# Optimization experiments

Measured on AMD Instinct MI355X. Metric: run time of the kernel, lower is better.

## Reference

```python
import jax, jax.numpy as jnp
import numpy as np

TOPK = 2
EPS = 1e-6  # RMSNorm epsilon


def setup_inputs() -> dict:
    key = jax.random.key(0)
    ks = jax.random.split(key, 8)
    b, t, d, h, n = 2, 1024, 1024, 2048, 16
    x = jax.random.normal(ks[0], (b, t, d), dtype=jnp.float32)
    router_w = jax.random.normal(ks[1], (n, d), dtype=jnp.float32) * (1.0 / np.sqrt(d))
    router_bias = jnp.zeros((n,), dtype=jnp.float32)
    bank_mag = jax.random.normal(ks[2], (n, d, h), dtype=jnp.float32) * (1.0 / np.sqrt(d))
    bank_freq = jax.random.uniform(ks[3], (n, d, h), dtype=jnp.float32, minval=0.5, maxval=2.0) * (1.0 / np.sqrt(d))
    bank_phase = jax.random.uniform(ks[4], (n, h), dtype=jnp.float32, minval=-0.3, maxval=0.3)
    bank_down = jax.random.normal(ks[5], (n, h, d), dtype=jnp.float32) * (1.0 / np.sqrt(h))
    norm_w = jnp.ones((d,), dtype=jnp.float32)
    return {
        'x': x, 'router_w': router_w, 'router_bias': router_bias,
        'bank_mag': bank_mag, 'bank_freq': bank_freq, 'bank_phase': bank_phase,
        'bank_down': bank_down, 'norm_w': norm_w,
    }


def reference(x, router_w, router_bias, bank_mag, bank_freq, bank_phase, bank_down, norm_w):
    b, t, d = x.shape
    # Router: scores [b,t,n], top-k selection, softmax over selected logits
    scores = jnp.einsum('btd,nd->btn', x, router_w) + router_bias
    topv, topi = jax.lax.top_k(scores, TOPK)            # [b,t,k]
    weights = jax.nn.softmax(topv, axis=-1)             # [b,t,k]

    fx = x.reshape(b * t, d)                            # [T,d]
    # Dense per-expert compute (mathematically identical to per-token gather+bmm):
    mag = jnp.einsum('td,ndh->tnh', fx, bank_mag)       # [T,n,h]
    freq = jnp.einsum('td,ndh->tnh', fx, bank_freq)     # [T,n,h]
    hidden = jnp.tanh(mag) * jnp.cos(jax.nn.softplus(freq) + 0.1 + bank_phase[None, :, :])
    out_all = jnp.einsum('tnh,nhd->tnd', hidden, bank_down)  # [T,n,d]

    # Gather the top-k expert outputs per token and combine with routing weights
    ti = topi.reshape(b * t, TOPK)                      # [T,k]
    sel = jnp.take_along_axis(out_all, ti[:, :, None], axis=1)  # [T,k,d]
    out = jnp.einsum('tkd,tk->td', sel, weights.reshape(b * t, TOPK)).reshape(b, t, d)

    # RMSNorm
    out = out * jax.lax.rsqrt(jnp.mean(out * out, axis=-1, keepdims=True) + EPS) * norm_w
    return out
```

## Files before the change

### kernel.cpp

```cpp
#include <hip/hip_runtime.h>
#include <hip/hip_bf16.h>
#include <cstdint>
#include <cstddef>

#define TT 2048
#define DD 1024
#define HH 2048
#define NE 16
#define WM128 48
#define BROW 17

typedef __bf16 bf16x8 __attribute__((ext_vector_type(8)));
typedef float f32x4 __attribute__((ext_vector_type(4)));

__device__ __forceinline__ unsigned short f2bf(float f) {
  union { float f; unsigned u; } v; v.f = f;
  unsigned r = (v.u + 0x7FFFu + ((v.u >> 16) & 1u)) >> 16;
  return (unsigned short)r;
}
__device__ __forceinline__ float bf2f(unsigned short s) {
  union { unsigned u; float f; } v; v.u = ((unsigned)s) << 16;
  return v.f;
}
__device__ __forceinline__ unsigned packbf(float lo, float hi) {
  return (unsigned)f2bf(lo) | ((unsigned)f2bf(hi) << 16);
}

__device__ __forceinline__ void gl_lds16(const void* g, void* l) {
  __builtin_amdgcn_global_load_lds(
      (const __attribute__((address_space(1))) unsigned int*)g,
      (__attribute__((address_space(3))) unsigned int*)l, 16, 0, 0);
}

union U4 { unsigned int u[4]; bf16x8 v; };

#define BARRIER_N(N)                                            \
  do {                                                          \
    asm volatile("s_waitcnt vmcnt(" #N ")" ::: "memory");       \
    asm volatile("s_waitcnt lgkmcnt(0)" ::: "memory");          \
    __builtin_amdgcn_sched_barrier(0);                          \
    __builtin_amdgcn_s_barrier();                               \
    __builtin_amdgcn_sched_barrier(0);                          \
  } while (0)

__global__ __launch_bounds__(256) void k_router(
    const float* __restrict__ x, const float* __restrict__ rw,
    const float* __restrict__ rb, int* __restrict__ cnt,
    int* __restrict__ list_tok, int* __restrict__ rec,
    float* __restrict__ wrec, unsigned short* __restrict__ xbf) {
  const int t = blockIdx.x;
  __shared__ float xs[DD];
  __shared__ float part[256];
  __shared__ float sc[NE];
  const float* xr = x + (size_t)t * DD;
  for (int i = threadIdx.x; i < DD; i += 256) xs[i] = xr[i];
  __syncthreads();
  {
    int i = threadIdx.x * 4;
    ushort4 o = { f2bf(xs[i]), f2bf(xs[i + 1]), f2bf(xs[i + 2]), f2bf(xs[i + 3]) };
    *reinterpret_cast<ushort4*>(xbf + (size_t)t * DD + i) = o;
  }
  const int e = threadIdx.x >> 4, j = threadIdx.x & 15;
  const float* w = rw + (size_t)e * DD;
  float s = 0.f;
  for (int i = j; i < DD; i += 16) s += xs[i] * w[i];
  part[threadIdx.x] = s;
  __syncthreads();
  if (threadIdx.x < NE) {
    float v = rb[threadIdx.x];
    #pragma unroll
    for (int q = 0; q < 16; ++q) v += part[threadIdx.x * 16 + q];
    sc[threadIdx.x] = v;
  }
  __syncthreads();
  if (threadIdx.x == 0) {
    int e1 = 0; float v1 = sc[0];
    #pragma unroll
    for (int q = 1; q < NE; ++q) { if (sc[q] > v1) { v1 = sc[q]; e1 = q; } }
    int e2 = -1; float v2 = -3.4e38f;
    #pragma unroll
    for (int q = 0; q < NE; ++q) {
      if (q != e1 && sc[q] > v2) { v2 = sc[q]; e2 = q; }
    }
    float ex = expf(v2 - v1);
    float w1 = 1.f / (1.f + ex);
    float w2 = ex / (1.f + ex);
    int p1 = atomicAdd(&cnt[e1], 1);
    int p2 = atomicAdd(&cnt[e2], 1);
    list_tok[e1 * TT + p1] = t;
    list_tok[e2 * TT + p2] = t;
    rec[t * 4 + 0] = e1; rec[t * 4 + 1] = p1;
    rec[t * 4 + 2] = e2; rec[t * 4 + 3] = p2;
    wrec[t * 2 + 0] = w1; wrec[t * 2 + 1] = w2;
  }
}

__global__ void k_sched(const int* __restrict__ cnt, int* __restrict__ work128,
                        int* __restrict__ woff) {
  if (threadIdx.x == 0) {
    int o = 0, n1 = 0;
    for (int e = 0; e < NE; ++e) {
      int ce = cnt[e];
      int a = (ce + 127) >> 7;
      for (int mb = 0; mb < a; ++mb) { work128[n1 * 2] = e; work128[n1 * 2 + 1] = mb; ++n1; }
      woff[e] = o; o += ce;
    }
    for (int q = n1; q < WM128; ++q) { work128[q * 2] = -1; work128[q * 2 + 1] = 0; }
  }
}

__global__ __launch_bounds__(256, 3) void k_up(
    const unsigned short* __restrict__ xbf,
    const float* __restrict__ bmag,
    const float* __restrict__ bfreq,
    const float* __restrict__ bphase,
    const int* __restrict__ cnt, const int* __restrict__ list_tok,
    const int* __restrict__ work, const int* __restrict__ woff,
    unsigned short* __restrict__ hid) {
  const int e = work[blockIdx.x * 2 + 0];
  if (e < 0) return;
  const int mt = work[blockIdx.x * 2 + 1];
  const int nt = blockIdx.y;
  const int ce = cnt[e];
  const int off = woff[e];
  __shared__ unsigned short As[2][128][32];
  __shared__ unsigned int BuM[2][64 * BROW];
  __shared__ unsigned int BuF[2][64 * BROW];
  __shared__ int toks[128];
  const int tid = threadIdx.x;
  if (tid < 128) {
    int r = mt * 128 + tid;
    toks[tid] = list_tok[e * TT + (r < ce ? r : ce - 1)];
  }
  __syncthreads();
  const int w = tid >> 6, l = tid & 63;
  size_t abase[2]; int aoff[2];
  #pragma unroll
  for (int p = 0; p < 2; ++p) {
    int row = p * 64 + w * 16 + (l >> 2);
    int g = (l & 3) ^ ((row >> 1) & 3);
    abase[p] = (size_t)toks[row] * DD + g * 8;
    aoff[p] = (p * 256 + w * 64 + l) * 8;
  }
  const int q2 = tid >> 4;
  const int b16 = tid & 15;
  const int n0 = nt * 64;
  const float* srcM = bmag  + (size_t)e * DD * HH + n0 + 4 * b16;
  const float* srcF = bfreq + (size_t)e * DD * HH + n0 + 4 * b16;
  int bwv[4];
  #pragma unroll
  for (int i = 0; i < 4; ++i) bwv[i] = (4 * b16 + i) * BROW + q2;

  const int wm = (w >> 1) * 64, wn = (w & 1) * 32;
  const int lr = l & 15, kg = l >> 4;
  const f32x4 zero = {0.f, 0.f, 0.f, 0.f};
  f32x4 accM[4][2], accF[4][2];
  #pragma unroll
  for (int a = 0; a < 4; ++a)
    #pragma unroll
    for (int b = 0; b < 2; ++b) { accM[a][b] = zero; accF[a][b] = zero; }

  float4 Am0, Am1, Af0, Af1;
  float4 Bm0, Bm1, Bf0, Bf1;

  auto glA = [&](int kt, int buf) {
    #pragma unroll
    for (int j = 0; j < 2; ++j)
      gl_lds16(xbf + abase[j] + kt * 32, &As[buf][0][0] + aoff[j]);
  };
  auto loadBA = [&](int kt) {
    const float* pM = srcM + (size_t)(kt * 32 + 2 * q2) * HH;
    const float* pF = srcF + (size_t)(kt * 32 + 2 * q2) * HH;
    Am0 = *reinterpret_cast<const float4*>(pM);
    Am1 = *reinterpret_cast<const float4*>(pM + HH);
    Af0 = *reinterpret_cast<const float4*>(pF);
    Af1 = *reinterpret_cast<const float4*>(pF + HH);
  };
  auto loadBB = [&](int kt) {
    const float* pM = srcM + (size_t)(kt * 32 + 2 * q2) * HH;
    const float* pF = srcF + (size_t)(kt * 32 + 2 * q2) * HH;
    Bm0 = *reinterpret_cast<const float4*>(pM);
    Bm1 = *reinterpret_cast<const float4*>(pM + HH);
    Bf0 = *reinterpret_cast<const float4*>(pF);
    Bf1 = *reinterpret_cast<const float4*>(pF + HH);
  };
  auto writeBA = [&](int buf) {
    const float* m0 = reinterpret_cast<const float*>(&Am0);
    const float* m1 = reinterpret_cast<const float*>(&Am1);
    const float* f0 = reinterpret_cast<const float*>(&Af0);
    const float* f1 = reinterpret_cast<const float*>(&Af1);
    #pragma unroll
    for (int i = 0; i < 4; ++i) {
      BuM[buf][bwv[i]] = packbf(m0[i], m1[i]);
      BuF[buf][bwv[i]] = packbf(f0[i], f1[i]);
    }
  };
  auto writeBB = [&](int buf) {
    const float* m0 = reinterpret_cast<const float*>(&Bm0);
    const float* m1 = reinterpret_cast<const float*>(&Bm1);
    const float* f0 = reinterpret_cast<const float*>(&Bf0);
    const float* f1 = reinterpret_cast<const float*>(&Bf1);
    #pragma unroll
    for (int i = 0; i < 4; ++i) {
      BuM[buf][bwv[i]] = packbf(m0[i], m1[i]);
      BuF[buf][bwv[i]] = packbf(f0[i], f1[i]);
    }
  };
  auto compute = [&](int buf) {
    bf16x8 av[4];
    #pragma unroll
    for (int fm = 0; fm < 4; ++fm) {
      int row = wm + fm * 16 + lr;
      int c = kg ^ ((row >> 1) & 3);
      av[fm] = *reinterpret_cast<const bf16x8*>(&As[buf][row][c * 8]);
    }
    U4 tm[2], tf[2];
    #pragma unroll
    for (int fn = 0; fn < 2; ++fn) {
      const int nb = (wn + fn * 16 + lr) * BROW + kg * 4;
      #pragma unroll
      for (int j2 = 0; j2 < 4; ++j2) {
        tm[fn].u[j2] = BuM[buf][nb + j2];
        tf[fn].u[j2] = BuF[buf][nb + j2];
      }
    }
    #pragma unroll
    for (int fm = 0; fm < 4; ++fm)
      #pragma unroll
      for (int fn = 0; fn < 2; ++fn) {
        accM[fm][fn] = __builtin_amdgcn_mfma_f32_16x16x32_bf16(av[fm], tm[fn].v, accM[fm][fn], 0, 0, 0);
        accF[fm][fn] = __builtin_amdgcn_mfma_f32_16x16x32_bf16(av[fm], tf[fn].v, accF[fm][fn], 0, 0, 0);
      }
  };

  glA(0, 0);
  __builtin_amdgcn_sched_barrier(0);
  loadBA(0);
  loadBB(1);
  writeBA(0);
  BARRIER_N(4);
  for (int kt = 0; kt < 32; kt += 2) {
    glA(kt + 1, 1);
    __builtin_amdgcn_sched_barrier(0);
    loadBA(kt + 2 < 32 ? kt + 2 : 31);
    compute(0);
    writeBB(1);
    BARRIER_N(4);
    const bool more = kt + 2 < 32;
    if (more) {
      glA(kt + 2, 0);
      __builtin_amdgcn_sched_barrier(0);
      loadBB(kt + 3 < 32 ? kt + 3 : 31);
    }
    compute(1);
    if (more) {
      writeBA(0);
      BARRIER_N(4);
    }
  }
  #pragma unroll
  for (int fn = 0; fn < 2; ++fn) {
    const int ng = n0 + wn + fn * 16 + lr;
    const float ph = bphase[e * HH + ng] + 0.1f;
    #pragma unroll
    for (int fm = 0; fm < 4; ++fm) {
      #pragma unroll
      for (int jj = 0; jj < 4; ++jj) {
        int m = mt * 128 + wm + fm * 16 + kg * 4 + jj;
        if (m < ce) {
          float mv = accM[fm][fn][jj];
          float fv = accF[fm][fn][jj];
          float exn = __expf(-fabsf(fv));
          float sp = fmaxf(fv, 0.f) + __logf(1.f + exn);
          float t2 = __expf(2.f * mv);
          float th = 1.f - 2.f / (t2 + 1.f);
          float hv = th * __cosf(sp + ph);
          hid[(size_t)(off + m) * HH + ng] = f2bf(hv);
        }
      }
    }
  }
}

__global__ __launch_bounds__(256, 4) void k_down(
    const unsigned short* __restrict__ hid,
    const float* __restrict__ bdown,
    const int* __restrict__ cnt,
    const int* __restrict__ work, const int* __restrict__ woff,
    unsigned short* __restrict__ op) {
  const int e = work[blockIdx.x * 2 + 0];
  if (e < 0) return;
  const int mt = work[blockIdx.x * 2 + 1];
  const int nt = blockIdx.y;
  const int ce = cnt[e];
  const int off = woff[e];
  __shared__ unsigned short As[2][128][32];
  __shared__ unsigned int Bu[2][64 * BROW];
  const int tid = threadIdx.x;
  const int w = tid >> 6, l = tid & 63;
  size_t abase[2]; int aoff[2];
  #pragma unroll
  for (int p = 0; p < 2; ++p) {
    int row = p * 64 + w * 16 + (l >> 2);
    int g = (l & 3) ^ ((row >> 1) & 3);
    int gr = mt * 128 + row; if (gr >= ce) gr = ce - 1;
    abase[p] = (size_t)(off + gr) * HH + g * 8;
    aoff[p] = (p * 256 + w * 64 + l) * 8;
  }
  const int q2 = tid >> 4;
  const int b16 = tid & 15;
  const int n0 = nt * 64;
  const float* srcD = bdown + (size_t)e * HH * DD + n0 + 4 * b16;
  int bwv[4];
  #pragma unroll
  for (int i = 0; i < 4; ++i) bwv[i] = (4 * b16 + i) * BROW + q2;

  const int wm = (w >> 1) * 64, wn = (w & 1) * 32;
  const int lr = l & 15, kg = l >> 4;
  const f32x4 zero = {0.f, 0.f, 0.f, 0.f};
  f32x4 acc[4][2];
  #pragma unroll
  for (int a = 0; a < 4; ++a)
    #pragma unroll
    for (int b = 0; b < 2; ++b) acc[a][b] = zero;

  float4 Ad0, Ad1;
  float4 Bd0, Bd1;

  auto glA = [&](int kt, int buf) {
    #pragma unroll
    for (int j = 0; j < 2; ++j)
      gl_lds16(hid + abase[j] + kt * 32, &As[buf][0][0] + aoff[j]);
  };
  auto loadBA = [&](int kt) {
    const float* pD = srcD + (size_t)(kt * 32 + 2 * q2) * DD;
    Ad0 = *reinterpret_cast<const float4*>(pD);
    Ad1 = *reinterpret_cast<const float4*>(pD + DD);
  };
  auto loadBB = [&](int kt) {
    const float* pD = srcD + (size_t)(kt * 32 + 2 * q2) * DD;
    Bd0 = *reinterpret_cast<const float4*>(pD);
    Bd1 = *reinterpret_cast<const float4*>(pD + DD);
  };
  auto writeBA = [&](int buf) {
    const float* d0 = reinterpret_cast<const float*>(&Ad0);
    const float* d1 = reinterpret_cast<const float*>(&Ad1);
    #pragma unroll
    for (int i = 0; i < 4; ++i) Bu[buf][bwv[i]] = packbf(d0[i], d1[i]);
  };
  auto writeBB = [&](int buf) {
    const float* d0 = reinterpret_cast<const float*>(&Bd0);
    const float* d1 = reinterpret_cast<const float*>(&Bd1);
    #pragma unroll
    for (int i = 0; i < 4; ++i) Bu[buf][bwv[i]] = packbf(d0[i], d1[i]);
  };
  auto compute = [&](int buf) {
    bf16x8 av[4];
    #pragma unroll
    for (int fm = 0; fm < 4; ++fm) {
      int row = wm + fm * 16 + lr;
      int c = kg ^ ((row >> 1) & 3);
      av[fm] = *reinterpret_cast<const bf16x8*>(&As[buf][row][c * 8]);
    }
    U4 t[2];
    #pragma unroll
    for (int fn = 0; fn < 2; ++fn) {
      const int nb = (wn + fn * 16 + lr) * BROW + kg * 4;
      #pragma unroll
      for (int j2 = 0; j2 < 4; ++j2) t[fn].u[j2] = Bu[buf][nb + j2];
    }
    #pragma unroll
    for (int fm = 0; fm < 4; ++fm)
      #pragma unroll
      for (int fn = 0; fn < 2; ++fn)
        acc[fm][fn] = __builtin_amdgcn_mfma_f32_16x16x32_bf16(av[fm], t[fn].v, acc[fm][fn], 0, 0, 0);
  };

  glA(0, 0);
  __builtin_amdgcn_sched_barrier(0);
  loadBA(0);
  loadBB(1);
  writeBA(0);
  BARRIER_N(2);
  for (int kt = 0; kt < 64; kt += 2) {
    glA(kt + 1, 1);
    __builtin_amdgcn_sched_barrier(0);
    loadBA(kt + 2 < 64 ? kt + 2 : 63);
    compute(0);
    writeBB(1);
    BARRIER_N(2);
    const bool more = kt + 2 < 64;
    if (more) {
      glA(kt + 2, 0);
      __builtin_amdgcn_sched_barrier(0);
      loadBB(kt + 3 < 64 ? kt + 3 : 63);
    }
    compute(1);
    if (more) {
      writeBA(0);
      BARRIER_N(2);
    }
  }
  #pragma unroll
  for (int fn = 0; fn < 2; ++fn) {
    const int ng = n0 + wn + fn * 16 + lr;
    #pragma unroll
    for (int fm = 0; fm < 4; ++fm) {
      #pragma unroll
      for (int jj = 0; jj < 4; ++jj) {
        int m = mt * 128 + wm + fm * 16 + kg * 4 + jj;
        if (m < ce)
          op[(size_t)(off + m) * DD + ng] = f2bf(acc[fm][fn][jj]);
      }
    }
  }
}

__global__ __launch_bounds__(256) void k_norm(
    const unsigned short* __restrict__ op, const int* __restrict__ woff,
    const int* __restrict__ rec, const float* __restrict__ wrec,
    const float* __restrict__ nw, float* __restrict__ out) {
  const int t = blockIdx.x;
  const int tid = threadIdx.x;
  __shared__ float red[4];
  const int e1 = rec[t * 4 + 0], p1 = rec[t * 4 + 1];
  const int e2 = rec[t * 4 + 2], p2 = rec[t * 4 + 3];
  const float w1 = wrec[t * 2 + 0], w2 = wrec[t * 2 + 1];
  const unsigned short* pa = op + (size_t)(woff[e1] + p1) * DD;
  const unsigned short* pb = op + (size_t)(woff[e2] + p2) * DD;
  float v[4]; float ss = 0.f;
  #pragma unroll
  for (int q = 0; q < 4; ++q) {
    int i = q * 256 + tid;
    v[q] = w1 * bf2f(pa[i]) + w2 * bf2f(pb[i]);
    ss += v[q] * v[q];
  }
  #pragma unroll
  for (int o = 32; o > 0; o >>= 1) ss += __shfl_xor(ss, o);
  if ((tid & 63) == 0) red[tid >> 6] = ss;
  __syncthreads();
  const float tot = red[0] + red[1] + red[2] + red[3];
  const float scl = rsqrtf(tot * (1.f / DD) + 1e-6f);
  #pragma unroll
  for (int q = 0; q < 4; ++q) {
    int i = q * 256 + tid;
    out[(size_t)t * DD + i] = v[q] * scl * nw[i];
  }
}

extern "C" void kernel_launch(void* const* d_in, const int* in_sizes, int n_in,
                              void* d_out, int out_size, void* d_ws, size_t ws_size,
                              hipStream_t stream) {
  const float* x      = (const float*)d_in[0];
  const float* rw     = (const float*)d_in[1];
  const float* rb     = (const float*)d_in[2];
  const float* bmag   = (const float*)d_in[3];
  const float* bfreq  = (const float*)d_in[4];
  const float* bphase = (const float*)d_in[5];
  const float* bdown  = (const float*)d_in[6];
  const float* nw     = (const float*)d_in[7];
  float* out = (float*)d_out;
  char* ws = (char*)d_ws;
  const size_t MB = 1024 * 1024;
  int*   cnt    = (int*)(ws + 0);
  int*   work1  = (int*)(ws + 128);
  int*   woff   = (int*)(ws + 2048);
  int*   list   = (int*)(ws + 4096);
  int*   rec    = (int*)(ws + 139264);
  float* wrec   = (float*)(ws + 172032);
  unsigned short* xbf = (unsigned short*)(ws + 1 * MB);
  unsigned short* hid = (unsigned short*)(ws + 5 * MB);
  unsigned short* op  = (unsigned short*)(ws + 21 * MB);

  hipMemsetAsync(cnt, 0, 64, stream);
  k_router<<<TT, 256, 0, stream>>>(x, rw, rb, cnt, list, rec, wrec, xbf);
  k_sched<<<1, 64, 0, stream>>>(cnt, work1, woff);
  k_up<<<dim3(WM128, HH / 64), 256, 0, stream>>>(xbf, bmag, bfreq, bphase,
                                                 cnt, list, work1, woff, hid);
  k_down<<<dim3(WM128, DD / 64), 256, 0, stream>>>(hid, bdown, cnt, work1, woff, op);
  k_norm<<<TT, 256, 0, stream>>>(op, woff, rec, wrec, nw, out);
}
```

Baseline: 293.2 us.

## Map expert tiles to XCDs so each expert's weights stay in one L2

Flattens the up and down projection grids to 1D and remaps block indices so that blocks with the same low three bits (which the hardware round-robins onto the same XCD) all work on one or two experts (e and e+8). Each expert's weight slices are then read through a single XCD's L2 instead of being spread across all eight, cutting redundant HBM traffic for the fp32 weight banks. A scheduler flag falls back to the old work-list mapping when some expert pair has too many row tiles to fit the fixed grid. The mapping relies on the round-robin dispatch of workgroups across XCDs and can cause load imbalance between XCDs when experts are uneven.

```diff
diff --git a/kernel.cpp b/kernel.cpp
--- a/kernel.cpp
+++ b/kernel.cpp
@@ -96,16 +96,42 @@
 }
 
 __global__ void k_sched(const int* __restrict__ cnt, int* __restrict__ work128,
-                        int* __restrict__ woff) {
+                        int* __restrict__ woff, int* __restrict__ nmb,
+                        int* __restrict__ flag) {
   if (threadIdx.x == 0) {
     int o = 0, n1 = 0;
     for (int e = 0; e < NE; ++e) {
       int ce = cnt[e];
       int a = (ce + 127) >> 7;
+      nmb[e] = a;
       for (int mb = 0; mb < a; ++mb) { work128[n1 * 2] = e; work128[n1 * 2 + 1] = mb; ++n1; }
       woff[e] = o; o += ce;
     }
     for (int q = n1; q < WM128; ++q) { work128[q * 2] = -1; work128[q * 2 + 1] = 0; }
+    int f = 0;
+    for (int xq = 0; xq < 8; ++xq)
+      if (nmb[xq] + nmb[xq + 8] > 6) f = 1;
+    flag[0] = f;
+  }
+}
+
+__device__ __forceinline__ bool xcd_map(int L, const int* nmb, const int* flag,
+                                        const int* work, int NTSH,
+                                        int& e, int& mt, int& nt) {
+  if (flag[0] == 0) {
+    int x = L & 7, r = L >> 3;
+    int m0 = nmb[x] << NTSH, m1 = nmb[x + 8] << NTSH;
+    if (r < m0) { e = x; mt = r >> NTSH; nt = r & ((1 << NTSH) - 1); return true; }
+    r -= m0;
+    if (r < m1) { e = x + 8; mt = r >> NTSH; nt = r & ((1 << NTSH) - 1); return true; }
+    return false;
+  } else {
+    int wq = L >> NTSH;
+    e = work[wq * 2];
+    if (e < 0) return false;
+    mt = work[wq * 2 + 1];
+    nt = L & ((1 << NTSH) - 1);
+    return true;
   }
 }
 
@@ -116,11 +142,10 @@
     const float* __restrict__ bphase,
     const int* __restrict__ cnt, const int* __restrict__ list_tok,
     const int* __restrict__ work, const int* __restrict__ woff,
+    const int* __restrict__ nmb, const int* __restrict__ flag,
     unsigned short* __restrict__ hid) {
-  const int e = work[blockIdx.x * 2 + 0];
-  if (e < 0) return;
-  const int mt = work[blockIdx.x * 2 + 1];
-  const int nt = blockIdx.y;
+  int e, mt, nt;
+  if (!xcd_map(blockIdx.x, nmb, flag, work, 5, e, mt, nt)) return;
   const int ce = cnt[e];
   const int off = woff[e];
   __shared__ unsigned short As[2][128][32];
@@ -287,11 +312,10 @@
     const float* __restrict__ bdown,
     const int* __restrict__ cnt,
     const int* __restrict__ work, const int* __restrict__ woff,
+    const int* __restrict__ nmb, const int* __restrict__ flag,
     unsigned short* __restrict__ op) {
-  const int e = work[blockIdx.x * 2 + 0];
-  if (e < 0) return;
-  const int mt = work[blockIdx.x * 2 + 1];
-  const int nt = blockIdx.y;
+  int e, mt, nt;
+  if (!xcd_map(blockIdx.x, nmb, flag, work, 4, e, mt, nt)) return;
   const int ce = cnt[e];
   const int off = woff[e];
   __shared__ unsigned short As[2][128][32];
@@ -465,6 +489,8 @@
   int*   cnt    = (int*)(ws + 0);
   int*   work1  = (int*)(ws + 128);
   int*   woff   = (int*)(ws + 2048);
+  int*   nmb    = (int*)(ws + 2176);
+  int*   flag   = (int*)(ws + 2304);
   int*   list   = (int*)(ws + 4096);
   int*   rec    = (int*)(ws + 139264);
   float* wrec   = (float*)(ws + 172032);
@@ -474,9 +500,9 @@
 
   hipMemsetAsync(cnt, 0, 64, stream);
   k_router<<<TT, 256, 0, stream>>>(x, rw, rb, cnt, list, rec, wrec, xbf);
-  k_sched<<<1, 64, 0, stream>>>(cnt, work1, woff);
-  k_up<<<dim3(WM128, HH / 64), 256, 0, stream>>>(xbf, bmag, bfreq, bphase,
-                                                 cnt, list, work1, woff, hid);
-  k_down<<<dim3(WM128, DD / 64), 256, 0, stream>>>(hid, bdown, cnt, work1, woff, op);
+  k_sched<<<1, 64, 0, stream>>>(cnt, work1, woff, nmb, flag);
+  k_up<<<WM128 * 32, 256, 0, stream>>>(xbf, bmag, bfreq, bphase,
+                                       cnt, list, work1, woff, nmb, flag, hid);
+  k_down<<<WM128 * 16, 256, 0, stream>>>(hid, bdown, cnt, work1, woff, nmb, flag, op);
   k_norm<<<TT, 256, 0, stream>>>(op, woff, rec, wrec, nw, out);
 }
```

New measurement: 263.2 us. 10.2% less time.

## Map expert M-tiles to XCDs via a balanced schedule table for L2 locality

Applied to the files above, without the earlier changes.

The scheduler now spreads the (expert, M-tile) work items across the 8 XCDs, always picking the least-loaded one, and records them in a per-XCD table. The up and down kernels use a 1D grid and decode blockIdx so that all N-tiles of one work item land on the same XCD and run back to back. The goal is that the shared token rows and expert weights are reused from that XCD's L2 instead of being fetched from memory again. The risk is that the greedy assignment spreads one expert's M-tiles over several XCDs, which limits reuse of the weight matrices, and that uneven group counts leave some XCDs idle.

```diff
diff --git a/kernel.cpp b/kernel.cpp
--- a/kernel.cpp
+++ b/kernel.cpp
@@ -95,18 +95,40 @@
   }
 }
 
-__global__ void k_sched(const int* __restrict__ cnt, int* __restrict__ work128,
-                        int* __restrict__ woff) {
+__global__ void k_sched(const int* __restrict__ cnt, int* __restrict__ woff,
+                        int* __restrict__ gtab, int* __restrict__ gcnt) {
   if (threadIdx.x == 0) {
-    int o = 0, n1 = 0;
+    int o = 0;
+    int gc[8];
+    #pragma unroll
+    for (int q = 0; q < 8; ++q) gc[q] = 0;
+    for (int q = 0; q < 64; ++q) gtab[q] = -1;
     for (int e = 0; e < NE; ++e) {
       int ce = cnt[e];
       int a = (ce + 127) >> 7;
-      for (int mb = 0; mb < a; ++mb) { work128[n1 * 2] = e; work128[n1 * 2 + 1] = mb; ++n1; }
+      for (int mb = 0; mb < a; ++mb) {
+        int x = 0;
+        #pragma unroll
+        for (int q = 1; q < 8; ++q) if (gc[q] < gc[x]) x = q;
+        gtab[x * 8 + gc[x]] = e * 256 + mb;
+        gc[x]++;
+      }
       woff[e] = o; o += ce;
     }
-    for (int q = n1; q < WM128; ++q) { work128[q * 2] = -1; work128[q * 2 + 1] = 0; }
-  }
+    #pragma unroll
+    for (int q = 0; q < 8; ++q) gcnt[q] = gc[q];
+  }
+}
+
+__device__ __forceinline__ bool xcd_map(int L, const int* gtab, const int* gcnt,
+                                        int NTSH, int& e, int& mt, int& nt) {
+  int x = L & 7, r = L >> 3;
+  int g = r >> NTSH;
+  if (g >= gcnt[x]) return false;
+  int v = gtab[x * 8 + g];
+  e = v >> 8; mt = v & 255;
+  nt = r & ((1 << NTSH) - 1);
+  return true;
 }
 
 __global__ __launch_bounds__(256, 3) void k_up(
@@ -115,12 +137,11 @@
     const float* __restrict__ bfreq,
     const float* __restrict__ bphase,
     const int* __restrict__ cnt, const int* __restrict__ list_tok,
-    const int* __restrict__ work, const int* __restrict__ woff,
+    const int* __restrict__ gtab, const int* __restrict__ gcnt,
+    const int* __restrict__ woff,
     unsigned short* __restrict__ hid) {
-  const int e = work[blockIdx.x * 2 + 0];
-  if (e < 0) return;
-  const int mt = work[blockIdx.x * 2 + 1];
-  const int nt = blockIdx.y;
+  int e, mt, nt;
+  if (!xcd_map(blockIdx.x, gtab, gcnt, 5, e, mt, nt)) return;
   const int ce = cnt[e];
   const int off = woff[e];
   __shared__ unsigned short As[2][128][32];
@@ -286,12 +307,11 @@
     const unsigned short* __restrict__ hid,
     const float* __restrict__ bdown,
     const int* __restrict__ cnt,
-    const int* __restrict__ work, const int* __restrict__ woff,
+    const int* __restrict__ gtab, const int* __restrict__ gcnt,
+    const int* __restrict__ woff,
     unsigned short* __restrict__ op) {
-  const int e = work[blockIdx.x * 2 + 0];
-  if (e < 0) return;
-  const int mt = work[blockIdx.x * 2 + 1];
-  const int nt = blockIdx.y;
+  int e, mt, nt;
+  if (!xcd_map(blockIdx.x, gtab, gcnt, 4, e, mt, nt)) return;
   const int ce = cnt[e];
   const int off = woff[e];
   __shared__ unsigned short As[2][128][32];
@@ -463,8 +483,9 @@
   char* ws = (char*)d_ws;
   const size_t MB = 1024 * 1024;
   int*   cnt    = (int*)(ws + 0);
-  int*   work1  = (int*)(ws + 128);
   int*   woff   = (int*)(ws + 2048);
+  int*   gtab   = (int*)(ws + 2176);
+  int*   gcnt   = (int*)(ws + 2432);
   int*   list   = (int*)(ws + 4096);
   int*   rec    = (int*)(ws + 139264);
   float* wrec   = (float*)(ws + 172032);
@@ -474,9 +495,9 @@
 
   hipMemsetAsync(cnt, 0, 64, stream);
   k_router<<<TT, 256, 0, stream>>>(x, rw, rb, cnt, list, rec, wrec, xbf);
-  k_sched<<<1, 64, 0, stream>>>(cnt, work1, woff);
-  k_up<<<dim3(WM128, HH / 64), 256, 0, stream>>>(xbf, bmag, bfreq, bphase,
-                                                 cnt, list, work1, woff, hid);
-  k_down<<<dim3(WM128, DD / 64), 256, 0, stream>>>(hid, bdown, cnt, work1, woff, op);
+  k_sched<<<1, 64, 0, stream>>>(cnt, woff, gtab, gcnt);
+  k_up<<<8 * 6 * 32, 256, 0, stream>>>(xbf, bmag, bfreq, bphase,
+                                       cnt, list, gtab, gcnt, woff, hid);
+  k_down<<<8 * 6 * 16, 256, 0, stream>>>(hid, bdown, cnt, gtab, gcnt, woff, op);
   k_norm<<<TT, 256, 0, stream>>>(op, woff, rec, wrec, nw, out);
 }
```

Result: no change. 293.9 us (+0.3%).
